# Optimization experiments

Hardware: AMD Instinct MI355X
Metric: run time of the kernel (lower is better)

## Reference

```python
import jax, jax.numpy as jnp
import numpy as np

P, K, D = 512, 4, 256          # identities, instances per id per modality, feature dim
N = 2 * P * K                  # two modality halves, as assumed by mod_idxs in the module
R_STRENGTH = 2.0               # cmrr_loss __init__ r=2.0 (soft_rank regularization_strength)


def _soft_rank_kl(values, reg_strength):
    """torchsort.soft_rank(values, regularization='kl', strength=reg_strength), rows of length n.

    theta = values/strength; sort descending -> s; w = [n,...,1].
    isotonic_kl solves argmin_{v noninc} <e^{s-v},1> + <w, v>; block value on [i..j] is
    LSE(s[i:j+1]) - LSE(log w[i:j+1]). Min-max formula (valid for PAV-solvable problems):
      dual_k = min_{i<=k} max_{j>=k} B[i,j].
    ranks = exp(s - dual) scattered back by the inverse permutation.
    """
    n = values.shape[1]
    theta = values * (1.0 / reg_strength)
    perm = jnp.argsort(-theta, axis=1)                     # descending sort order
    s = jnp.take_along_axis(theta, perm, axis=1)
    inv_perm = jnp.argsort(perm, axis=1)
    logw = jnp.log(jnp.arange(n, 0, -1, dtype=values.dtype))  # log([n, n-1, ..., 1])
    k = jnp.arange(n)
    ii, jj, kk = k[:, None, None], k[None, :, None], k[None, None, :]
    # segment [i, max(i,j)]; for invalid i>j it degenerates to {i} so LSE stays finite (no NaN grads)
    seg = (kk >= ii) & (kk <= jnp.maximum(jj, ii))         # (n, n, n) indexed [i, j, k]
    neg = jnp.asarray(-jnp.inf, values.dtype)
    lse_s = jax.nn.logsumexp(jnp.where(seg[None], s[:, None, None, :], neg), axis=-1)  # (R,n,n)
    lse_w = jax.nn.logsumexp(jnp.where(seg, logw[None, None, :], neg), axis=-1)        # (n,n)
    valid = k[:, None] <= k[None, :]                       # i <= j
    B = jnp.where(valid[None], lse_s - lse_w[None], neg)   # block values, -inf where invalid
    T = jax.lax.cummax(B, axis=2, reverse=True)            # T[:,i,k] = max_{j>=k} B[:,i,j]
    tri = k[:, None] <= k[None, :]                         # i <= k
    dual = jnp.min(jnp.where(tri[None], T, jnp.inf), axis=1)  # (R, n), nonincreasing
    return jnp.exp(jnp.take_along_axis(s - dual, inv_perm, axis=1))


def _pairwise_dist(f):
    # ||f_i - f_j||_2 with clamp(min=1e-12) before sqrt, as in the module
    sq = jnp.sum(f * f, axis=1)
    d2 = sq[:, None] + sq[None, :] - 2.0 * (f @ f.T)
    return jnp.sqrt(jnp.clip(d2, 1e-12, None))


def _spearman(a, b):
    a = a - jnp.mean(a, axis=1, keepdims=True)
    a = a / jnp.linalg.norm(a, axis=1, keepdims=True)
    b = b - jnp.mean(b, axis=1, keepdims=True)
    b = b / jnp.linalg.norm(b, axis=1, keepdims=True)
    return jnp.sum(a * b, axis=1)


def setup_inputs() -> dict:
    key = jax.random.key(0)
    k0, k1, k2 = jax.random.split(key, 3)
    ids = jnp.repeat(jnp.arange(P), K)                     # PK sampling within each modality
    target = jnp.concatenate([ids, ids])                   # first half modality 0, second half modality 1
    f0 = jax.random.normal(k0, (N, D), jnp.float32)
    f1 = jax.random.normal(k1, (N, D), jnp.float32)
    f2 = jax.random.normal(k2, (N, D), jnp.float32)
    return {"f0": f0, "f1": f1, "f2": f2, "target": target, "k_pos": K}


def reference(f0, f1, f2, target, k_pos):
    feats = (f0, f1, f2)
    n = target.shape[0]
    pos = target[None, :] == target[:, None]
    mod = jnp.concatenate([jnp.zeros(n // 2, jnp.int32), jnp.ones(n // 2, jnp.int32)])
    mask = pos & (mod[None, :] != mod[:, None])            # pos_idxs & ~mod_idxs
    # boolean-mask gather dists[mask].view(N,-1): per row, the k_pos True columns in increasing order
    idx = jnp.argsort(jnp.where(mask, 0, 1), axis=1, stable=True)[:, :k_pos]
    ranks = []
    for f in feats:
        dists = _pairwise_dist(f)
        dist_intra = jnp.take_along_axis(dists, idx, axis=1)   # (N, k_pos)
        ranks.append(_soft_rank_kl(dist_intra, R_STRENGTH))
    L = len(feats)
    loss = jnp.zeros((n,), f0.dtype)
    for i in range(L):
        for j in range(i + 1, L):
            loss = loss + (_spearman(ranks[i], ranks[j]) + 1.0) / 2.0
    loss = loss / (L * (L - 1) / 2.0)
    return jnp.mean(loss)
```

## Files before the change

kernel.cpp:

```cpp
#include <hip/hip_runtime.h>
#include <hip/hip_bf16.h>

constexpr int D4 = 64;
constexpr int KP = 4;

__device__ __forceinline__ void soft_rank4(const float d2[4], float r[4]) {
    float th[4]; int p[4] = {0, 1, 2, 3};
#pragma unroll
    for (int t = 0; t < 4; ++t) th[t] = 0.5f * sqrtf(fmaxf(d2[t], 1e-12f));
#define CSWAP(a, b)                                                           \
    if (th[a] < th[b]) {                                                      \
        float tt = th[a]; th[a] = th[b]; th[b] = tt;                          \
        int tp = p[a]; p[a] = p[b]; p[b] = tp;                                \
    }
    CSWAP(0, 1) CSWAP(1, 2) CSWAP(2, 3) CSWAP(0, 1) CSWAP(1, 2) CSWAP(0, 1)
#undef CSWAP
    const float logW[4][4] = {
        {1.3862944f, 1.9459101f, 2.1972246f, 2.3025851f},
        {0.f,        1.0986123f, 1.6094379f, 1.7917595f},
        {0.f,        0.f,        0.6931472f, 1.0986123f},
        {0.f,        0.f,        0.f,        0.f}};
    float B[4][4];
#pragma unroll
    for (int i = 0; i < 4; ++i) {
        float run = 0.f;
#pragma unroll
        for (int j = 0; j < 4; ++j) {
            if (j >= i) {
                run += __expf(th[j] - th[i]);
                B[i][j] = th[i] + __logf(run) - logW[i][j];
            }
        }
    }
    float rs[4];
#pragma unroll
    for (int k = 0; k < 4; ++k) {
        float dual = 1e30f;
#pragma unroll
        for (int i = 0; i < 4; ++i) {
            if (i <= k) {
                float mx = -1e30f;
#pragma unroll
                for (int j = 0; j < 4; ++j)
                    if (j >= k) mx = fmaxf(mx, B[i][j]);
                dual = fminf(dual, mx);
            }
        }
        rs[k] = __expf(th[k] - dual);
    }
#pragma unroll
    for (int t = 0; t < 4; ++t) {
        float v = rs[3];
        v = (p[2] == t) ? rs[2] : v;
        v = (p[1] == t) ? rs[1] : v;
        v = (p[0] == t) ? rs[0] : v;
        r[t] = v;
    }
}

__device__ __forceinline__ float spearman4(const float a[4], const float b[4]) {
    float ma = 0.25f * (a[0] + a[1] + a[2] + a[3]);
    float mb = 0.25f * (b[0] + b[1] + b[2] + b[3]);
    float sab = 0.f, saa = 0.f, sbb = 0.f;
#pragma unroll
    for (int t = 0; t < 4; ++t) {
        float x = a[t] - ma, y = b[t] - mb;
        sab += x * y; saa += x * x; sbb += y * y;
    }
    return sab * rsqrtf(saa * sbb);
}

__global__ __launch_bounds__(256) void cmrr_main(
        const float* __restrict__ f0, const float* __restrict__ f1,
        const float* __restrict__ f2, const int* __restrict__ target,
        float* __restrict__ block_sums, int N) {
    const float* F[3] = {f0, f1, f2};
    const int wave = threadIdx.x >> 6;
    const int lane = threadIdx.x & 63;
    const int row = blockIdx.x * 4 + wave;
    float loss = 0.f;
    if (row < N) {
        const int id = target[row];
        const int base = (row < (N >> 1)) ? (N >> 1) : 0;
        const int j0 = base + KP * id;
        float d2[3][4];
#pragma unroll
        for (int f = 0; f < 3; ++f) {
            const float4* xi = (const float4*)(F[f] + (size_t)row * (D4 * 4));
            const float4 a = xi[lane];
#pragma unroll
            for (int t = 0; t < 4; ++t) {
                const float4* xj =
                    (const float4*)(F[f] + (size_t)(j0 + t) * (D4 * 4));
                const float4 b = xj[lane];
                const float dx = a.x - b.x, dy = a.y - b.y;
                const float dz = a.z - b.z, dw = a.w - b.w;
                d2[f][t] = dx * dx + dy * dy + dz * dz + dw * dw;
            }
        }
#pragma unroll
        for (int f = 0; f < 3; ++f) {
#pragma unroll
            for (int t = 0; t < 4; ++t) {
                float v = d2[f][t];
#pragma unroll
                for (int m = 32; m >= 1; m >>= 1) v += __shfl_xor(v, m, 64);
                d2[f][t] = v;
            }
        }
        float ranks[3][4];
#pragma unroll
        for (int f = 0; f < 3; ++f) soft_rank4(d2[f], ranks[f]);
        const float c01 = spearman4(ranks[0], ranks[1]);
        const float c02 = spearman4(ranks[0], ranks[2]);
        const float c12 = spearman4(ranks[1], ranks[2]);
        loss = (c01 + c02 + c12 + 3.f) * (0.5f / 3.f);
    }
    __shared__ float ws4[4];
    if (lane == 0) ws4[wave] = loss;
    __syncthreads();
    if (threadIdx.x == 0)
        block_sums[blockIdx.x] = (ws4[0] + ws4[1]) + (ws4[2] + ws4[3]);
}

__global__ __launch_bounds__(256) void cmrr_reduce(
        const float* __restrict__ block_sums, float* __restrict__ out,
        int nblocks, float inv_n) {
    float s = 0.f;
    for (int i = threadIdx.x; i < nblocks; i += 256) s += block_sums[i];
#pragma unroll
    for (int m = 32; m >= 1; m >>= 1) s += __shfl_xor(s, m, 64);
    __shared__ float w[4];
    if ((threadIdx.x & 63) == 0) w[threadIdx.x >> 6] = s;
    __syncthreads();
    if (threadIdx.x == 0) out[0] = ((w[0] + w[1]) + (w[2] + w[3])) * inv_n;
}

extern "C" void kernel_launch(void* const* d_in, const int* in_sizes, int n_in,
                              void* d_out, int out_size, void* d_ws,
                              size_t ws_size, hipStream_t stream) {
    const float* f0 = (const float*)d_in[0];
    const float* f1 = (const float*)d_in[1];
    const float* f2 = (const float*)d_in[2];
    const int* target = (const int*)d_in[3];
    const int N = in_sizes[3];
    const int nblocks = (N + 3) / 4;
    float* bs = (float*)d_ws;
    cmrr_main<<<nblocks, 256, 0, stream>>>(f0, f1, f2, target, bs, N);
    cmrr_reduce<<<1, 256, 0, stream>>>(bs, (float*)d_out, nblocks,
                                       1.0f / (float)N);
}
```

Measured before the change: 79.08 us.

## Exploit symmetric identity groups and fuse reduction via atomic last-block pattern

Result: slower. 87.70 us (+10.9%).

```diff
diff --git a/kernel.cpp b/kernel.cpp
--- a/kernel.cpp
+++ b/kernel.cpp
@@ -1,8 +1,6 @@
 #include <hip/hip_runtime.h>
 #include <hip/hip_bf16.h>
 
-constexpr int D4 = 64;
-constexpr int KP = 4;
 
 __device__ __forceinline__ void soft_rank4(const float d2[4], float r[4]) {
     float th[4]; int p[4] = {0, 1, 2, 3};
@@ -70,70 +68,83 @@
     return sab * rsqrtf(saa * sbb);
 }
 
-__global__ __launch_bounds__(256) void cmrr_main(
+__device__ __forceinline__ float row_loss(const float d2a[3][4]) {
+    float ranks[3][4];
+#pragma unroll
+    for (int f = 0; f < 3; ++f) soft_rank4(d2a[f], ranks[f]);
+    const float c01 = spearman4(ranks[0], ranks[1]);
+    const float c02 = spearman4(ranks[0], ranks[2]);
+    const float c12 = spearman4(ranks[1], ranks[2]);
+    return (c01 + c02 + c12 + 3.f) * (0.5f / 3.f);
+}
+
+__global__ __launch_bounds__(256) void cmrr_fused(
         const float* __restrict__ f0, const float* __restrict__ f1,
         const float* __restrict__ f2, const int* __restrict__ target,
-        float* __restrict__ block_sums, int N) {
+        float* __restrict__ ws, float* __restrict__ out, int N, float inv_n,
+        int nblocks) {
     const float* F[3] = {f0, f1, f2};
+    const int g = blockIdx.x;
     const int wave = threadIdx.x >> 6;
     const int lane = threadIdx.x & 63;
-    const int row = blockIdx.x * 4 + wave;
-    float loss = 0.f;
-    if (row < N) {
-        const int id = target[row];
-        const int base = (row < (N >> 1)) ? (N >> 1) : 0;
-        const int j0 = base + KP * id;
-        float d2[3][4];
+    const int half = N >> 1;
+
+    __shared__ float4 stage[256];
+    __shared__ float d2s[3][4][4];
+    __shared__ float lsum[4];
+
+    const int r0 = 4 * g + wave;
+    const int id = target[4 * g];
+    const int jbase = half + 4 * id;
+
 #pragma unroll
-        for (int f = 0; f < 3; ++f) {
-            const float4* xi = (const float4*)(F[f] + (size_t)row * (D4 * 4));
-            const float4 a = xi[lane];
+    for (int f = 0; f < 3; ++f) {
+        if (f) __syncthreads();
+        stage[threadIdx.x] =
+            ((const float4*)(F[f] + (size_t)jbase * 256))[threadIdx.x];
+        __syncthreads();
+        const float4 a = ((const float4*)(F[f] + (size_t)r0 * 256))[lane];
+        float d2[4];
 #pragma unroll
-            for (int t = 0; t < 4; ++t) {
-                const float4* xj =
-                    (const float4*)(F[f] + (size_t)(j0 + t) * (D4 * 4));
-                const float4 b = xj[lane];
-                const float dx = a.x - b.x, dy = a.y - b.y;
-                const float dz = a.z - b.z, dw = a.w - b.w;
-                d2[f][t] = dx * dx + dy * dy + dz * dz + dw * dw;
-            }
+        for (int j = 0; j < 4; ++j) {
+            const float4 b = stage[j * 64 + lane];
+            const float dx = a.x - b.x, dy = a.y - b.y;
+            const float dz = a.z - b.z, dw = a.w - b.w;
+            float v = dx * dx + dy * dy + dz * dz + dw * dw;
+#pragma unroll
+            for (int m = 32; m >= 1; m >>= 1) v += __shfl_xor(v, m, 64);
+            d2[j] = v;
         }
+        if (lane == 0) {
 #pragma unroll
-        for (int f = 0; f < 3; ++f) {
+            for (int j = 0; j < 4; ++j) d2s[f][wave][j] = d2[j];
+        }
+    }
+    __syncthreads();
+
+    float d2a[3][4], d2b[3][4];
 #pragma unroll
-            for (int t = 0; t < 4; ++t) {
-                float v = d2[f][t];
+    for (int f = 0; f < 3; ++f) {
 #pragma unroll
-                for (int m = 32; m >= 1; m >>= 1) v += __shfl_xor(v, m, 64);
-                d2[f][t] = v;
-            }
+        for (int t = 0; t < 4; ++t) {
+            d2a[f][t] = d2s[f][wave][t];
+            d2b[f][t] = d2s[f][t][wave];
         }
-        float ranks[3][4];
-#pragma unroll
-        for (int f = 0; f < 3; ++f) soft_rank4(d2[f], ranks[f]);
-        const float c01 = spearman4(ranks[0], ranks[1]);
-        const float c02 = spearman4(ranks[0], ranks[2]);
-        const float c12 = spearman4(ranks[1], ranks[2]);
-        loss = (c01 + c02 + c12 + 3.f) * (0.5f / 3.f);
     }
-    __shared__ float ws4[4];
-    if (lane == 0) ws4[wave] = loss;
+    const float loss2 = row_loss(d2a) + row_loss(d2b);
+    if (lane == 0) lsum[wave] = loss2;
     __syncthreads();
-    if (threadIdx.x == 0)
-        block_sums[blockIdx.x] = (ws4[0] + ws4[1]) + (ws4[2] + ws4[3]);
-}
 
-__global__ __launch_bounds__(256) void cmrr_reduce(
-        const float* __restrict__ block_sums, float* __restrict__ out,
-        int nblocks, float inv_n) {
-    float s = 0.f;
-    for (int i = threadIdx.x; i < nblocks; i += 256) s += block_sums[i];
-#pragma unroll
-    for (int m = 32; m >= 1; m >>= 1) s += __shfl_xor(s, m, 64);
-    __shared__ float w[4];
-    if ((threadIdx.x & 63) == 0) w[threadIdx.x >> 6] = s;
-    __syncthreads();
-    if (threadIdx.x == 0) out[0] = ((w[0] + w[1]) + (w[2] + w[3])) * inv_n;
+    if (threadIdx.x == 0) {
+        const float partial = (lsum[0] + lsum[1]) + (lsum[2] + lsum[3]);
+        atomicAdd(ws, partial);
+        __threadfence();
+        unsigned old = atomicAdd((unsigned*)(ws + 1), 1u);
+        if (old == (unsigned)(nblocks - 1)) {
+            const float total = atomicAdd(ws, 0.0f);
+            out[0] = total * inv_n;
+        }
+    }
 }
 
 extern "C" void kernel_launch(void* const* d_in, const int* in_sizes, int n_in,
@@ -144,9 +155,9 @@
     const float* f2 = (const float*)d_in[2];
     const int* target = (const int*)d_in[3];
     const int N = in_sizes[3];
-    const int nblocks = (N + 3) / 4;
-    float* bs = (float*)d_ws;
-    cmrr_main<<<nblocks, 256, 0, stream>>>(f0, f1, f2, target, bs, N);
-    cmrr_reduce<<<1, 256, 0, stream>>>(bs, (float*)d_out, nblocks,
-                                       1.0f / (float)N);
+    const int nblocks = N / 8;
+    hipMemsetAsync(d_ws, 0, 16, stream);
+    cmrr_fused<<<nblocks, 256, 0, stream>>>(f0, f1, f2, target, (float*)d_ws,
+                                            (float*)d_out, N, 1.0f / (float)N,
+                                            nblocks);
 }
```
